# Performance work log

Measured on AMD Instinct MI355X. Metric: run time of the kernel, lower is better.

Reference implementation:

```python
import jax, jax.numpy as jnp
import numpy as np

D_MODEL = 16
D_STATE = 16
D_CONV = 4
EXPAND = 2
D_INNER = EXPAND * D_MODEL  # 32
DT_RANK = 1                 # ceil(d_model / 16)
H_MLP = 2 * D_MODEL         # MLP hidden = input_dim * 2
EPS = 1e-6
B, L = 16, 8192


def setup_inputs() -> dict:
    key = jax.random.key(0)
    ks = jax.random.split(key, 20)
    g = lambda i, shape, s: jax.random.normal(ks[i], shape, jnp.float32) * s
    # S4D-real init for A_log, as in mamba_ssm
    A_log = jnp.log(jnp.broadcast_to(jnp.arange(1, D_STATE + 1, dtype=jnp.float32), (D_INNER, D_STATE)))
    return {
        "x": jax.random.normal(ks[0], (B, L, D_MODEL), jnp.float32),
        "rms1_w": jnp.ones((D_MODEL,), jnp.float32),
        "in_proj_w": g(1, (D_MODEL, 2 * D_INNER), 0.25),
        "conv_w": g(2, (D_INNER, D_CONV), 0.3),
        "conv_b": g(3, (D_INNER,), 0.05),
        "x_proj_w": g(4, (D_INNER, DT_RANK + 2 * D_STATE), 0.2),
        "dt_proj_w": g(5, (DT_RANK, D_INNER), 0.5),
        "dt_proj_b": g(6, (D_INNER,), 0.1),
        "A_log": A_log,
        "D_skip": jnp.ones((D_INNER,), jnp.float32),
        "out_proj_w": g(7, (D_INNER, D_MODEL), 0.2),
        "rms2_w": jnp.ones((D_MODEL,), jnp.float32),
        "fc1_w": g(8, (D_MODEL, H_MLP), 0.25),
        "fc1_b": g(9, (H_MLP,), 0.05),
        "fc2_w": g(10, (H_MLP, H_MLP), 0.2),
        "fc2_b": g(11, (H_MLP,), 0.05),
        "fc3_w": g(12, (H_MLP, D_MODEL), 0.2),
        "fc3_b": g(13, (D_MODEL,), 0.05),
    }


def _rmsnorm(h, w):
    v = jnp.mean(h.astype(jnp.float32) ** 2, axis=-1, keepdims=True)
    return w * (h * jax.lax.rsqrt(v + EPS))


def _mamba(x0, in_proj_w, conv_w, conv_b, x_proj_w, dt_proj_w, dt_proj_b, A_log, D_skip, out_proj_w):
    b, l, _ = x0.shape
    xz = x0 @ in_proj_w                      # [B,L,2*Di]
    xm, z = jnp.split(xz, 2, axis=-1)        # each [B,L,Di]
    # causal depthwise conv1d (kernel D_CONV), padding d_conv-1, truncated to L
    xp = jnp.pad(xm, ((0, 0), (D_CONV - 1, 0), (0, 0)))
    xc = conv_b + sum(conv_w[:, k] * xp[:, k:k + l, :] for k in range(D_CONV))
    xc = jax.nn.silu(xc)
    # input-dependent dt, B, C
    proj = xc @ x_proj_w                     # [B,L,dt_rank+2*Ds]
    dt, Bm, Cm = jnp.split(proj, [DT_RANK, DT_RANK + D_STATE], axis=-1)
    dt = jax.nn.softplus(dt @ dt_proj_w + dt_proj_b)   # [B,L,Di]
    A = -jnp.exp(A_log)                      # [Di,Ds]
    deltaA = jnp.exp(dt[..., None] * A)                             # [B,L,Di,Ds]
    deltaBx = dt[..., None] * Bm[:, :, None, :] * xc[..., None]     # [B,L,Di,Ds]
    # sequential selective scan over time (time-major for lax.scan)
    def step(h, inputs):
        dA, dBx, C = inputs                  # [B,Di,Ds],[B,Di,Ds],[B,Ds]
        h = dA * h + dBx
        y = jnp.einsum('bds,bs->bd', h, C)
        return h, y
    h0 = jnp.zeros((b, D_INNER, D_STATE), xc.dtype)
    xs = (deltaA.transpose(1, 0, 2, 3), deltaBx.transpose(1, 0, 2, 3), Cm.transpose(1, 0, 2))
    _, ys = jax.lax.scan(step, h0, xs)       # [L,B,Di]
    y = ys.transpose(1, 0, 2) + D_skip * xc  # [B,L,Di]
    y = y * jax.nn.silu(z)
    return y @ out_proj_w                    # [B,L,Dm]


def reference(x, rms1_w, in_proj_w, conv_w, conv_b, x_proj_w, dt_proj_w, dt_proj_b,
              A_log, D_skip, out_proj_w, rms2_w, fc1_w, fc1_b, fc2_w, fc2_b, fc3_w, fc3_b):
    x0 = _rmsnorm(x, rms1_w)
    x1 = _mamba(x0, in_proj_w, conv_w, conv_b, x_proj_w, dt_proj_w, dt_proj_b, A_log, D_skip, out_proj_w)
    x = x1 + x
    x2 = _rmsnorm(x, rms2_w)
    h = jax.nn.relu(x2 @ fc1_w + fc1_b)
    h = jax.nn.relu(h @ fc2_w + fc2_b)
    x3 = h @ fc3_w + fc3_b
    return x + x3
```

## Files before the change

### kernel.cpp

```cpp
#include <hip/hip_runtime.h>

#define LSEQ 8192
#define NBAT 16
#define DMOD 16
#define DINN 32
#define DSTA 16
#define CL   32
#define NCH  (LSEQ / CL)
#define NCHT (NBAT * NCH)
#define NROWS (NBAT * LSEQ)
#define SUMN ((size_t)NCHT * 512)
#define NSEG 8
#define SEGC (NCH / NSEG)
#define RECU 800
#define LOG2E 1.44269504f

typedef __attribute__((ext_vector_type(8))) short bf16x8;
typedef __attribute__((ext_vector_type(4))) float f32x4;

__device__ __forceinline__ float fsilu(float v) { return v / (1.f + __expf(-v)); }
__device__ __forceinline__ float fsoftplus(float v) {
  return v > 20.f ? v : __logf(1.f + __expf(v));
}
__device__ __forceinline__ unsigned packbf(float a, float b) {
  unsigned r;
  asm("v_cvt_pk_bf16_f32 %0, %1, %2" : "=v"(r) : "v"(a), "v"(b));
  return r;
}
__device__ __forceinline__ short f2bf(float f) {
  return (short)(packbf(f, f) & 0xffffu);
}
__device__ __forceinline__ float bf2f(short s) {
  union { unsigned u; float f; } v;
  v.u = ((unsigned)(unsigned short)s) << 16;
  return v.f;
}
__device__ __forceinline__ float bflo(unsigned u) {
  union { unsigned a; float f; } v; v.a = u << 16; return v.f;
}
__device__ __forceinline__ float bfhi(unsigned u) {
  union { unsigned a; float f; } v; v.a = u & 0xffff0000u; return v.f;
}

__device__ __forceinline__ void load_x_row(const float* __restrict__ x, long r,
                                           float* __restrict__ xr) {
  const float4* xp = reinterpret_cast<const float4*>(x + r * DMOD);
  float4 v0 = xp[0], v1 = xp[1], v2 = xp[2], v3 = xp[3];
  xr[0] = v0.x; xr[1] = v0.y; xr[2] = v0.z; xr[3] = v0.w;
  xr[4] = v1.x; xr[5] = v1.y; xr[6] = v1.z; xr[7] = v1.w;
  xr[8] = v2.x; xr[9] = v2.y; xr[10] = v2.z; xr[11] = v2.w;
  xr[12] = v3.x; xr[13] = v3.y; xr[14] = v3.z; xr[15] = v3.w;
}

__device__ __forceinline__ f32x4 mm(bf16x8 a, bf16x8 b, f32x4 c) {
  return __builtin_amdgcn_mfma_f32_16x16x32_bf16(a, b, c, 0, 0, 0);
}
__device__ __forceinline__ bf16x8 bfrag(const float* __restrict__ W, int ldw,
                                        int coloff, int col, int kg, int kreal) {
  bf16x8 b = {0, 0, 0, 0, 0, 0, 0, 0};
#pragma unroll
  for (int e = 0; e < 8; e++) {
    int k = kg * 8 + e;
    if (k < kreal) b[e] = f2bf(W[k * ldw + coloff + col]);
  }
  return b;
}

__global__ __launch_bounds__(256) void k_prep(
    const float* __restrict__ x, const float* __restrict__ rms1w,
    const float* __restrict__ ipw, const float* __restrict__ cw,
    const float* __restrict__ cb, const float* __restrict__ xpw,
    const float* __restrict__ dtw, const float* __restrict__ dtb,
    const float* __restrict__ A_log, const float* __restrict__ Dskip,
    unsigned* __restrict__ rec, float* __restrict__ Pb,
    float* __restrict__ Hb) {
  __shared__ short xmv[67][36];
  __shared__ short x0b[64][40];
  __shared__ short xcb[64][40];
  int t = threadIdx.x;
  int lane = t & 63, wid = t >> 6;
  int col = lane & 15, kg = lane >> 4;
  long row0 = (long)blockIdx.x * 64;
  int l0 = (int)(row0 & (LSEQ - 1));
  const f32x4 zero4 = {0.f, 0.f, 0.f, 0.f};

  bf16x8 Bip0 = bfrag(ipw, 64, 0, col, kg, 16);
  bf16x8 Bip1 = bfrag(ipw, 64, 16, col, kg, 16);
  bf16x8 Bdt, Bb, Bc;
#pragma unroll
  for (int e = 0; e < 8; e++) {
    int k = kg * 8 + e;
    Bdt[e] = (col == 0) ? f2bf(xpw[k * 33]) : (short)0;
    Bb[e] = f2bf(xpw[k * 33 + 1 + col]);
    Bc[e] = f2bf(xpw[k * 33 + 17 + col]);
  }

  if (t < 128) {
    int row = t >> 1, hf = t & 1;
    const float4* xp =
        reinterpret_cast<const float4*>(x + (row0 + row) * DMOD + hf * 8);
    float4 v0 = xp[0], v1 = xp[1];
    float xr[8] = {v0.x, v0.y, v0.z, v0.w, v1.x, v1.y, v1.z, v1.w};
    float ss = 0.f;
#pragma unroll
    for (int i = 0; i < 8; i++) ss += xr[i] * xr[i];
    ss += __shfl_xor(ss, 1);
    float inv1 = rsqrtf(ss * (1.f / 16.f) + 1e-6f);
    unsigned u[4];
#pragma unroll
    for (int i = 0; i < 4; i++)
      u[i] = packbf(xr[2 * i] * inv1 * rms1w[hf * 8 + 2 * i],
                    xr[2 * i + 1] * inv1 * rms1w[hf * 8 + 2 * i + 1]);
    *reinterpret_cast<uint4*>(&x0b[row][hf * 8]) =
        make_uint4(u[0], u[1], u[2], u[3]);
  } else if (t < 224) {
    int h = (t - 128) >> 5, k = (t - 128) & 31;
    short v = 0;
    if (l0 != 0) {
      float xr[16];
      load_x_row(x, row0 - 3 + h, xr);
      float ss = 0.f;
#pragma unroll
      for (int i = 0; i < 16; i++) ss += xr[i] * xr[i];
      float inv1 = rsqrtf(ss * (1.f / 16.f) + 1e-6f);
      float acc = 0.f;
#pragma unroll
      for (int i = 0; i < 16; i++)
        acc = fmaf(xr[i] * inv1 * rms1w[i], ipw[i * 64 + k], acc);
      v = f2bf(acc);
    }
    xmv[h][k] = v;
  }
  __syncthreads();

  {
    int arow = wid * 16 + col;
    bf16x8 a = {0, 0, 0, 0, 0, 0, 0, 0};
    if (kg < 2) a = *reinterpret_cast<const bf16x8*>(&x0b[arow][kg * 8]);
    f32x4 m0 = mm(a, Bip0, zero4);
    f32x4 m1 = mm(a, Bip1, zero4);
    int orow = 3 + wid * 16 + kg * 4;
#pragma unroll
    for (int reg = 0; reg < 4; reg++) {
      unsigned p = packbf(m0[reg], m1[reg]);
      xmv[orow + reg][col] = (short)(p & 0xffffu);
      xmv[orow + reg][col + 16] = (short)(p >> 16);
    }
  }
  __syncthreads();

  {
    int row = t >> 2, q = t & 3;
    unsigned u[4];
#pragma unroll
    for (int dp = 0; dp < 4; dp++) {
      int d = q * 8 + dp * 2;
      float ce = cb[d], co = cb[d + 1];
#pragma unroll
      for (int k = 0; k < 4; k++) {
        unsigned xu = *reinterpret_cast<const unsigned*>(&xmv[row + k][d]);
        ce = fmaf(cw[d * 4 + k], bflo(xu), ce);
        co = fmaf(cw[(d + 1) * 4 + k], bfhi(xu), co);
      }
      u[dp] = packbf(fsilu(ce), fsilu(co));
    }
    *reinterpret_cast<uint4*>(&xcb[row][q * 8]) =
        make_uint4(u[0], u[1], u[2], u[3]);
  }
  __syncthreads();

  {
    int arow = wid * 16 + col;
    bf16x8 a2 = *reinterpret_cast<const bf16x8*>(&xcb[arow][kg * 8]);
    f32x4 pd = mm(a2, Bdt, zero4);
    f32x4 pb = mm(a2, Bb, zero4);
    f32x4 pc = mm(a2, Bc, zero4);
    int orow = wid * 16 + kg * 4;
#pragma unroll
    for (int reg = 0; reg < 4; reg++) {
      unsigned p = packbf(pb[reg], pc[reg]);
      xmv[orow + reg][col] = (short)(p & 0xffffu);
      xmv[orow + reg][16 + col] = (short)(p >> 16);
      if (col == 0) xmv[orow + reg][32] = f2bf(pd[reg]);
    }
  }
  __syncthreads();

  {
    int row = t >> 2, q = t & 3;
    float p0 = bf2f(xmv[row][32]);
    unsigned u[4];
#pragma unroll
    for (int dp = 0; dp < 4; dp++) {
      int d = q * 8 + dp * 2;
      u[dp] = packbf(fsoftplus(fmaf(p0, dtw[d], dtb[d])),
                     fsoftplus(fmaf(p0, dtw[d + 1], dtb[d + 1])));
    }
    *reinterpret_cast<uint4*>(&x0b[row][q * 8]) =
        make_uint4(u[0], u[1], u[2], u[3]);
  }
  __syncthreads();

  {
    int ch = t >> 7, b128 = t & 127;
    int d = b128 >> 2, s4 = (b128 & 3) << 2;
    float Ad0 = -__expf(A_log[d * 16 + s4 + 0]) * LOG2E;
    float Ad1 = -__expf(A_log[d * 16 + s4 + 1]) * LOG2E;
    float Ad2 = -__expf(A_log[d * 16 + s4 + 2]) * LOG2E;
    float Ad3 = -__expf(A_log[d * 16 + s4 + 3]) * LOG2E;
    float dskd = Dskip[d];
    bool w0 = (t & 3) == 0;
    float H0 = 0.f, H1 = 0.f, H2 = 0.f, H3 = 0.f, cum = 0.f;
#pragma unroll 4
    for (int li = 0; li < CL; li++) {
      int row = ch * CL + li;
      float dt = bf2f(x0b[row][d]);
      float xcv = bf2f(xcb[row][d]);
      float dx = dt * xcv;
      cum += dt;
      uint2 bu = *reinterpret_cast<const uint2*>(&xmv[row][s4]);
      uint2 cu = *reinterpret_cast<const uint2*>(&xmv[row][16 + s4]);
      float a;
      a = __builtin_amdgcn_exp2f(dt * Ad0); H0 = fmaf(a, H0, dx * bflo(bu.x));
      a = __builtin_amdgcn_exp2f(dt * Ad1); H1 = fmaf(a, H1, dx * bfhi(bu.x));
      a = __builtin_amdgcn_exp2f(dt * Ad2); H2 = fmaf(a, H2, dx * bflo(bu.y));
      a = __builtin_amdgcn_exp2f(dt * Ad3); H3 = fmaf(a, H3, dx * bfhi(bu.y));
      float py = bflo(cu.x) * H0;
      py = fmaf(bfhi(cu.x), H1, py);
      py = fmaf(bflo(cu.y), H2, py);
      py = fmaf(bfhi(cu.y), H3, py);
      py += __shfl_xor(py, 1);
      py += __shfl_xor(py, 2);
      if (w0) xcb[row][d] = f2bf(fmaf(dskd, xcv, py));
    }
    size_t sb_ = (size_t)(blockIdx.x * 2 + ch) * 512 + (size_t)(d * 16 + s4);
    *reinterpret_cast<float4*>(Pb + sb_) = make_float4(
        __builtin_amdgcn_exp2f(cum * Ad0), __builtin_amdgcn_exp2f(cum * Ad1),
        __builtin_amdgcn_exp2f(cum * Ad2), __builtin_amdgcn_exp2f(cum * Ad3));
    *reinterpret_cast<float4*>(Hb + sb_) = make_float4(H0, H1, H2, H3);
  }
  __syncthreads();

  {
    unsigned* rb0 = rec + (size_t)(blockIdx.x * 2) * RECU;
#pragma unroll
    for (int i = 0; i < 7; i++) {
      int idx = i * 256 + t;
      if (idx < 1600) {
        int ch = idx / 800;
        int rem = idx - ch * 800;
        int c = rem >> 5, l = rem & 31;
        int row = ch * 32 + l;
        unsigned val;
        if (c < 16)
          val = *reinterpret_cast<const unsigned*>(&xcb[row][2 * c]);
        else if (c < 24)
          val = *reinterpret_cast<const unsigned*>(&xmv[row][16 + 2 * (c - 16)]);
        else
          val = (unsigned)(unsigned short)xmv[row][32];
        rb0[ch * RECU + rem] = val;
      }
    }
  }
}

__global__ __launch_bounds__(256) void k_seg(float* __restrict__ Pb,
                                             float* __restrict__ Hb,
                                             float* __restrict__ segP,
                                             float* __restrict__ segH) {
  int g = blockIdx.x * 256 + threadIdx.x;
  int b = g >> 12;
  int rem = g & 4095;
  int seg = rem >> 9, st = rem & 511;
  size_t o = ((size_t)(b * NCH + seg * SEGC)) * 512 + st;
  float h = 0.f, p = 1.f;
#pragma unroll 4
  for (int c = 0; c < SEGC; c++) {
    float P = Pb[o], H = Hb[o];
    Pb[o] = p;
    Hb[o] = h;
    h = fmaf(P, h, H);
    p *= P;
    o += 512;
  }
  size_t so = (size_t)(b * NSEG + seg) * 512 + st;
  segP[so] = p;
  segH[so] = h;
}

__global__ __launch_bounds__(256) void k_carry(const float* __restrict__ segP,
                                               const float* __restrict__ segH,
                                               float* __restrict__ carry) {
  int g = blockIdx.x * 256 + threadIdx.x;
  int b = g >> 9, st = g & 511;
  float h = 0.f;
#pragma unroll
  for (int s = 0; s < NSEG; s++) {
    size_t so = (size_t)(b * NSEG + s) * 512 + st;
    carry[so] = h;
    h = fmaf(segP[so], h, segH[so]);
  }
}

__global__ __launch_bounds__(256) void k_mlp(
    const unsigned* __restrict__ rec, const float* __restrict__ x,
    const float* __restrict__ A_log, const float* __restrict__ Pb,
    const float* __restrict__ Hb, const float* __restrict__ carry,
    const float* __restrict__ dtw, const float* __restrict__ dtb,
    const float* __restrict__ rms1w, const float* __restrict__ ipw,
    const float* __restrict__ opw, const float* __restrict__ rms2w,
    const float* __restrict__ f1w, const float* __restrict__ f1b,
    const float* __restrict__ f2w, const float* __restrict__ f2b,
    const float* __restrict__ f3w, const float* __restrict__ f3b,
    float* __restrict__ out) {
  __shared__ float h0L[4 * 516];
  __shared__ float Ads[512];
  __shared__ short sbx[128][24];
  __shared__ short sby[128][40];
  int t = threadIdx.x, bc = blockIdx.x;
  long row0 = (long)bc * 128;

  Ads[t] = -__expf(A_log[t]) * LOG2E;
  Ads[256 + t] = -__expf(A_log[256 + t]) * LOG2E;
#pragma unroll
  for (int i = 0; i < 8; i++) {
    int idx = i * 256 + t;
    int chl = idx >> 9, st = idx & 511;
    int gc = bc * 4 + chl;
    size_t o = (size_t)gc * 512 + st;
    int b = gc >> 8, seg = (gc >> 5) & 7;
    h0L[chl * 516 + st] =
        fmaf(Pb[o], carry[(size_t)(b * NSEG + seg) * 512 + st], Hb[o]);
  }
  {
    int row = t >> 1, hf = t & 1;
    const float4* xp =
        reinterpret_cast<const float4*>(x + (row0 + row) * DMOD + hf * 8);
    float4 v0 = xp[0], v1 = xp[1];
    float xr[8] = {v0.x, v0.y, v0.z, v0.w, v1.x, v1.y, v1.z, v1.w};
    float ss = 0.f;
#pragma unroll
    for (int i = 0; i < 8; i++) ss += xr[i] * xr[i];
    ss += __shfl_xor(ss, 1);
    float inv1 = rsqrtf(ss * (1.f / 16.f) + 1e-6f);
    unsigned u[4];
#pragma unroll
    for (int i = 0; i < 4; i++)
      u[i] = packbf(xr[2 * i] * inv1 * rms1w[hf * 8 + 2 * i],
                    xr[2 * i + 1] * inv1 * rms1w[hf * 8 + 2 * i + 1]);
    *reinterpret_cast<uint4*>(&sbx[t >> 1][hf * 8]) =
        make_uint4(u[0], u[1], u[2], u[3]);
  }
  __syncthreads();

  {
    int ch = t >> 6, half = (t >> 5) & 1, l = t & 31;
    const unsigned* rb = rec + (size_t)(bc * 4 + ch) * RECU;
    float Cv[16];
#pragma unroll
    for (int c = 0; c < 8; c++) {
      unsigned u = rb[(16 + c) * 32 + l];
      Cv[2 * c] = bflo(u);
      Cv[2 * c + 1] = bfhi(u);
    }
    float p0 = bflo(rb[24 * 32 + l]);
    const float* h0c = &h0L[ch * 516];
    int row = ch * 32 + l;
#pragma unroll
    for (int cc = 0; cc < 8; cc++) {
      int c = half * 8 + cc;
      int d0 = 2 * c, d1 = 2 * c + 1;
      float cd0 = fsoftplus(fmaf(p0, dtw[d0], dtb[d0]));
      float cd1 = fsoftplus(fmaf(p0, dtw[d1], dtb[d1]));
#pragma unroll
      for (int dl = 1; dl < 32; dl <<= 1) {
        float u0 = __shfl_up(cd0, dl, 32);
        float u1 = __shfl_up(cd1, dl, 32);
        if (l >= dl) { cd0 += u0; cd1 += u1; }
      }
      unsigned yu = rb[c * 32 + l];
      float acc0 = bflo(yu), acc1 = bfhi(yu);
      int dof0 = d0 * 16, dof1 = d1 * 16;
#pragma unroll
      for (int s = 0; s < 16; s++) {
        float e0 = __builtin_amdgcn_exp2f(Ads[dof0 + s] * cd0);
        float e1 = __builtin_amdgcn_exp2f(Ads[dof1 + s] * cd1);
        acc0 = fmaf(e0 * Cv[s], h0c[dof0 + s], acc0);
        acc1 = fmaf(e1 * Cv[s], h0c[dof1 + s], acc1);
      }
      *reinterpret_cast<unsigned*>(&sby[row][2 * c]) = packbf(acc0, acc1);
    }
  }
  __syncthreads();

  {
    int lane = t & 63, w = t >> 6;
    int col = lane & 15, kg = lane >> 4;
    bf16x8 Bz0 = bfrag(ipw + 32, 64, 0, col, kg, 16);
    bf16x8 Bz1 = bfrag(ipw + 32, 64, 16, col, kg, 16);
    bf16x8 Bop = bfrag(opw, 16, 0, col, kg, 32);
    bf16x8 Bf1_0 = bfrag(f1w, 32, 0, col, kg, 16);
    bf16x8 Bf1_1 = bfrag(f1w, 32, 16, col, kg, 16);
    bf16x8 Bf2_0 = bfrag(f2w, 32, 0, col, kg, 32);
    bf16x8 Bf2_1 = bfrag(f2w, 32, 16, col, kg, 32);
    bf16x8 Bf3 = bfrag(f3w, 16, 0, col, kg, 32);
    float b1_0 = f1b[col], b1_1 = f1b[16 + col];
    float b2_0 = f2b[col], b2_1 = f2b[16 + col];
    float b3c = f3b[col], rw2 = rms2w[col];
    const f32x4 zero4 = {0.f, 0.f, 0.f, 0.f};
#pragma unroll 1
    for (int rt = 0; rt < 2; rt++) {
      int tile0 = w * 32 + rt * 16;
      bf16x8 ax0 = {0, 0, 0, 0, 0, 0, 0, 0};
      if (kg < 2) ax0 = *reinterpret_cast<const bf16x8*>(&sbx[tile0 + col][kg * 8]);
      f32x4 zf0 = mm(ax0, Bz0, zero4);
      f32x4 zf1 = mm(ax0, Bz1, zero4);
#pragma unroll
      for (int reg = 0; reg < 4; reg++) {
        int lrow = tile0 + kg * 4 + reg;
        float y0 = bf2f(sby[lrow][col]);
        float y1 = bf2f(sby[lrow][16 + col]);
        unsigned p = packbf(y0 * fsilu(zf0[reg]), y1 * fsilu(zf1[reg]));
        sby[lrow][col] = (short)(p & 0xffffu);
        sby[lrow][16 + col] = (short)(p >> 16);
      }
      bf16x8 ayo = *reinterpret_cast<const bf16x8*>(&sby[tile0 + col][kg * 8]);
      f32x4 x1f = mm(ayo, Bop, zero4);
      float xres[4];
#pragma unroll
      for (int reg = 0; reg < 4; reg++) {
        long grow = row0 + tile0 + kg * 4 + reg;
        xres[reg] = x1f[reg] + x[grow * 16 + col];
      }
#pragma unroll
      for (int reg = 0; reg < 4; reg++) {
        float ss = xres[reg] * xres[reg];
        ss += __shfl_xor(ss, 1);
        ss += __shfl_xor(ss, 2);
        ss += __shfl_xor(ss, 4);
        ss += __shfl_xor(ss, 8);
        float inv2 = rsqrtf(ss * (1.f / 16.f) + 1e-6f);
        sby[tile0 + kg * 4 + reg][col] = f2bf(xres[reg] * inv2 * rw2);
      }
      bf16x8 ax2 = {0, 0, 0, 0, 0, 0, 0, 0};
      if (kg < 2) ax2 = *reinterpret_cast<const bf16x8*>(&sby[tile0 + col][kg * 8]);
      f32x4 h1f0 = mm(ax2, Bf1_0, zero4);
      f32x4 h1f1 = mm(ax2, Bf1_1, zero4);
#pragma unroll
      for (int reg = 0; reg < 4; reg++) {
        int lrow = tile0 + kg * 4 + reg;
        unsigned p = packbf(fmaxf(h1f0[reg] + b1_0, 0.f),
                            fmaxf(h1f1[reg] + b1_1, 0.f));
        sby[lrow][col] = (short)(p & 0xffffu);
        sby[lrow][16 + col] = (short)(p >> 16);
      }
      bf16x8 ah1 = *reinterpret_cast<const bf16x8*>(&sby[tile0 + col][kg * 8]);
      f32x4 h2f0 = mm(ah1, Bf2_0, zero4);
      f32x4 h2f1 = mm(ah1, Bf2_1, zero4);
#pragma unroll
      for (int reg = 0; reg < 4; reg++) {
        int lrow = tile0 + kg * 4 + reg;
        unsigned p = packbf(fmaxf(h2f0[reg] + b2_0, 0.f),
                            fmaxf(h2f1[reg] + b2_1, 0.f));
        sby[lrow][col] = (short)(p & 0xffffu);
        sby[lrow][16 + col] = (short)(p >> 16);
      }
      bf16x8 ah2 = *reinterpret_cast<const bf16x8*>(&sby[tile0 + col][kg * 8]);
      f32x4 x3f = mm(ah2, Bf3, zero4);
#pragma unroll
      for (int reg = 0; reg < 4; reg++) {
        long grow = row0 + tile0 + kg * 4 + reg;
        out[grow * 16 + col] = xres[reg] + x3f[reg] + b3c;
      }
    }
  }
}

extern "C" void kernel_launch(void* const* d_in, const int* in_sizes, int n_in,
                              void* d_out, int out_size, void* d_ws,
                              size_t ws_size, hipStream_t stream) {
  const float* x = (const float*)d_in[0];
  const float* rms1w = (const float*)d_in[1];
  const float* ipw = (const float*)d_in[2];
  const float* cw = (const float*)d_in[3];
  const float* cb = (const float*)d_in[4];
  const float* xpw = (const float*)d_in[5];
  const float* dtw = (const float*)d_in[6];
  const float* dtb = (const float*)d_in[7];
  const float* A_log = (const float*)d_in[8];
  const float* Dskip = (const float*)d_in[9];
  const float* opw = (const float*)d_in[10];
  const float* rms2w = (const float*)d_in[11];
  const float* f1w = (const float*)d_in[12];
  const float* f1b = (const float*)d_in[13];
  const float* f2w = (const float*)d_in[14];
  const float* f2b = (const float*)d_in[15];
  const float* f3w = (const float*)d_in[16];
  const float* f3b = (const float*)d_in[17];
  float* out = (float*)d_out;

  unsigned* rec = (unsigned*)d_ws;
  float* Pb = (float*)(rec + (size_t)NCHT * RECU);
  float* Hb = Pb + SUMN;
  float* segP = Hb + SUMN;
  float* segH = segP + NBAT * NSEG * 512;
  float* carry = segH + NBAT * NSEG * 512;

  hipLaunchKernelGGL(k_prep, dim3(NROWS / 64), dim3(256), 0, stream, x, rms1w,
                     ipw, cw, cb, xpw, dtw, dtb, A_log, Dskip, rec, Pb, Hb);
  hipLaunchKernelGGL(k_seg, dim3(256), dim3(256), 0, stream, Pb, Hb, segP,
                     segH);
  hipLaunchKernelGGL(k_carry, dim3(32), dim3(256), 0, stream, segP, segH,
                     carry);
  hipLaunchKernelGGL(k_mlp, dim3(NROWS / 128), dim3(256), 0, stream, rec, x,
                     A_log, Pb, Hb, carry, dtw, dtb, rms1w, ipw, opw, rms2w,
                     f1w, f1b, f2w, f2b, f3w, f3b, out);
}
```

Measured before the change: 84.67 us.

## Make each wavefront own one chunk so block barriers become compiler fences

k_prep and k_mlp are restructured so every 64-lane wavefront processes its own 32-row chunk in private shared-memory slices. Most __syncthreads barriers become compiler-only memory fences, relying on in-wave lockstep execution. The scan gives each lane 8 states instead of 4, which halves the shuffle reduction but doubles per-lane serial work. The k_prep grid is halved, and the change risks lower parallelism in the scan plus correctness that depends on wave-synchronous LDS ordering.

```diff
diff --git a/kernel.cpp b/kernel.cpp
--- a/kernel.cpp
+++ b/kernel.cpp
@@ -14,6 +14,7 @@
 #define SEGC (NCH / NSEG)
 #define RECU 800
 #define LOG2E 1.44269504f
+#define FENCE() asm volatile("" ::: "memory")
 
 typedef __attribute__((ext_vector_type(8))) short bf16x8;
 typedef __attribute__((ext_vector_type(4))) float f32x4;
@@ -74,14 +75,15 @@
     const float* __restrict__ A_log, const float* __restrict__ Dskip,
     unsigned* __restrict__ rec, float* __restrict__ Pb,
     float* __restrict__ Hb) {
-  __shared__ short xmv[67][36];
-  __shared__ short x0b[64][40];
-  __shared__ short xcb[64][40];
+  __shared__ short XM[4][35][36];
+  __shared__ short X0[4][32][32];
+  __shared__ short XC[4][32][40];
   int t = threadIdx.x;
-  int lane = t & 63, wid = t >> 6;
-  int col = lane & 15, kg = lane >> 4;
-  long row0 = (long)blockIdx.x * 64;
-  int l0 = (int)(row0 & (LSEQ - 1));
+  int l = t & 63, wid = t >> 6;
+  int col = l & 15, kg = l >> 4;
+  int chunk = blockIdx.x * 4 + wid;
+  long row0 = (long)chunk * CL;
+  bool first = (chunk & (NCH - 1)) == 0;
   const f32x4 zero4 = {0.f, 0.f, 0.f, 0.f};
 
   bf16x8 Bip0 = bfrag(ipw, 64, 0, col, kg, 16);
@@ -95,8 +97,8 @@
     Bc[e] = f2bf(xpw[k * 33 + 17 + col]);
   }
 
-  if (t < 128) {
-    int row = t >> 1, hf = t & 1;
+  {
+    int row = l >> 1, hf = l & 1;
     const float4* xp =
         reinterpret_cast<const float4*>(x + (row0 + row) * DMOD + hf * 8);
     float4 v0 = xp[0], v1 = xp[1];
@@ -111,154 +113,174 @@
     for (int i = 0; i < 4; i++)
       u[i] = packbf(xr[2 * i] * inv1 * rms1w[hf * 8 + 2 * i],
                     xr[2 * i + 1] * inv1 * rms1w[hf * 8 + 2 * i + 1]);
-    *reinterpret_cast<uint4*>(&x0b[row][hf * 8]) =
+    *reinterpret_cast<uint4*>(&X0[wid][row][hf * 8]) =
         make_uint4(u[0], u[1], u[2], u[3]);
-  } else if (t < 224) {
-    int h = (t - 128) >> 5, k = (t - 128) & 31;
-    short v = 0;
-    if (l0 != 0) {
+  }
+  if (l < 48) {
+    int h = l >> 4, k2 = (l & 15) * 2;
+    float a0 = 0.f, a1 = 0.f;
+    if (!first) {
       float xr[16];
       load_x_row(x, row0 - 3 + h, xr);
       float ss = 0.f;
 #pragma unroll
       for (int i = 0; i < 16; i++) ss += xr[i] * xr[i];
       float inv1 = rsqrtf(ss * (1.f / 16.f) + 1e-6f);
-      float acc = 0.f;
-#pragma unroll
-      for (int i = 0; i < 16; i++)
-        acc = fmaf(xr[i] * inv1 * rms1w[i], ipw[i * 64 + k], acc);
-      v = f2bf(acc);
-    }
-    xmv[h][k] = v;
-  }
-  __syncthreads();
-
-  {
-    int arow = wid * 16 + col;
+#pragma unroll
+      for (int i = 0; i < 16; i++) {
+        float x0i = xr[i] * inv1 * rms1w[i];
+        a0 = fmaf(x0i, ipw[i * 64 + k2], a0);
+        a1 = fmaf(x0i, ipw[i * 64 + k2 + 1], a1);
+      }
+    }
+    *reinterpret_cast<unsigned*>(&XM[wid][h][k2]) = packbf(a0, a1);
+  }
+  FENCE();
+
+#pragma unroll
+  for (int rt = 0; rt < 2; rt++) {
+    int arow = rt * 16 + col;
     bf16x8 a = {0, 0, 0, 0, 0, 0, 0, 0};
-    if (kg < 2) a = *reinterpret_cast<const bf16x8*>(&x0b[arow][kg * 8]);
+    if (kg < 2) a = *reinterpret_cast<const bf16x8*>(&X0[wid][arow][kg * 8]);
     f32x4 m0 = mm(a, Bip0, zero4);
     f32x4 m1 = mm(a, Bip1, zero4);
-    int orow = 3 + wid * 16 + kg * 4;
+    int orow = 3 + rt * 16 + kg * 4;
 #pragma unroll
     for (int reg = 0; reg < 4; reg++) {
       unsigned p = packbf(m0[reg], m1[reg]);
-      xmv[orow + reg][col] = (short)(p & 0xffffu);
-      xmv[orow + reg][col + 16] = (short)(p >> 16);
-    }
-  }
-  __syncthreads();
-
-  {
-    int row = t >> 2, q = t & 3;
-    unsigned u[4];
-#pragma unroll
-    for (int dp = 0; dp < 4; dp++) {
-      int d = q * 8 + dp * 2;
+      XM[wid][orow + reg][col] = (short)(p & 0xffffu);
+      XM[wid][orow + reg][col + 16] = (short)(p >> 16);
+    }
+  }
+  FENCE();
+
+  {
+    int row = l >> 1, hf = l & 1;
+    unsigned u[8];
+#pragma unroll
+    for (int dp = 0; dp < 8; dp++) {
+      int d = hf * 16 + dp * 2;
       float ce = cb[d], co = cb[d + 1];
 #pragma unroll
       for (int k = 0; k < 4; k++) {
-        unsigned xu = *reinterpret_cast<const unsigned*>(&xmv[row + k][d]);
+        unsigned xu = *reinterpret_cast<const unsigned*>(&XM[wid][row + k][d]);
         ce = fmaf(cw[d * 4 + k], bflo(xu), ce);
         co = fmaf(cw[(d + 1) * 4 + k], bfhi(xu), co);
       }
       u[dp] = packbf(fsilu(ce), fsilu(co));
     }
-    *reinterpret_cast<uint4*>(&xcb[row][q * 8]) =
+    *reinterpret_cast<uint4*>(&XC[wid][row][hf * 16]) =
         make_uint4(u[0], u[1], u[2], u[3]);
-  }
-  __syncthreads();
-
-  {
-    int arow = wid * 16 + col;
-    bf16x8 a2 = *reinterpret_cast<const bf16x8*>(&xcb[arow][kg * 8]);
+    *reinterpret_cast<uint4*>(&XC[wid][row][hf * 16 + 8]) =
+        make_uint4(u[4], u[5], u[6], u[7]);
+  }
+  FENCE();
+
+#pragma unroll
+  for (int rt = 0; rt < 2; rt++) {
+    int arow = rt * 16 + col;
+    bf16x8 a2 = *reinterpret_cast<const bf16x8*>(&XC[wid][arow][kg * 8]);
     f32x4 pd = mm(a2, Bdt, zero4);
     f32x4 pb = mm(a2, Bb, zero4);
     f32x4 pc = mm(a2, Bc, zero4);
-    int orow = wid * 16 + kg * 4;
+    int orow = 3 + rt * 16 + kg * 4;
 #pragma unroll
     for (int reg = 0; reg < 4; reg++) {
       unsigned p = packbf(pb[reg], pc[reg]);
-      xmv[orow + reg][col] = (short)(p & 0xffffu);
-      xmv[orow + reg][16 + col] = (short)(p >> 16);
-      if (col == 0) xmv[orow + reg][32] = f2bf(pd[reg]);
-    }
-  }
-  __syncthreads();
-
-  {
-    int row = t >> 2, q = t & 3;
-    float p0 = bf2f(xmv[row][32]);
-    unsigned u[4];
-#pragma unroll
-    for (int dp = 0; dp < 4; dp++) {
-      int d = q * 8 + dp * 2;
+      XM[wid][orow + reg][col] = (short)(p & 0xffffu);
+      XM[wid][orow + reg][16 + col] = (short)(p >> 16);
+      if (col == 0) XM[wid][orow + reg][32] = f2bf(pd[reg]);
+    }
+  }
+  FENCE();
+
+  {
+    int row = l >> 1, hf = l & 1;
+    float p0 = bf2f(XM[wid][3 + row][32]);
+    unsigned u[8];
+#pragma unroll
+    for (int dp = 0; dp < 8; dp++) {
+      int d = hf * 16 + dp * 2;
       u[dp] = packbf(fsoftplus(fmaf(p0, dtw[d], dtb[d])),
                      fsoftplus(fmaf(p0, dtw[d + 1], dtb[d + 1])));
     }
-    *reinterpret_cast<uint4*>(&x0b[row][q * 8]) =
+    *reinterpret_cast<uint4*>(&X0[wid][row][hf * 16]) =
         make_uint4(u[0], u[1], u[2], u[3]);
-  }
-  __syncthreads();
-
-  {
-    int ch = t >> 7, b128 = t & 127;
-    int d = b128 >> 2, s4 = (b128 & 3) << 2;
-    float Ad0 = -__expf(A_log[d * 16 + s4 + 0]) * LOG2E;
-    float Ad1 = -__expf(A_log[d * 16 + s4 + 1]) * LOG2E;
-    float Ad2 = -__expf(A_log[d * 16 + s4 + 2]) * LOG2E;
-    float Ad3 = -__expf(A_log[d * 16 + s4 + 3]) * LOG2E;
+    *reinterpret_cast<uint4*>(&X0[wid][row][hf * 16 + 8]) =
+        make_uint4(u[4], u[5], u[6], u[7]);
+  }
+  FENCE();
+
+  {
+    int d = l >> 1, sh = (l & 1) * 8;
+    float4 alo = *reinterpret_cast<const float4*>(A_log + d * DSTA + sh);
+    float4 ahi = *reinterpret_cast<const float4*>(A_log + d * DSTA + sh + 4);
+    float Ad[8] = {-__expf(alo.x) * LOG2E, -__expf(alo.y) * LOG2E,
+                   -__expf(alo.z) * LOG2E, -__expf(alo.w) * LOG2E,
+                   -__expf(ahi.x) * LOG2E, -__expf(ahi.y) * LOG2E,
+                   -__expf(ahi.z) * LOG2E, -__expf(ahi.w) * LOG2E};
     float dskd = Dskip[d];
-    bool w0 = (t & 3) == 0;
-    float H0 = 0.f, H1 = 0.f, H2 = 0.f, H3 = 0.f, cum = 0.f;
+    float H[8] = {0.f, 0.f, 0.f, 0.f, 0.f, 0.f, 0.f, 0.f};
+    float cum = 0.f;
+    bool wy = (l & 1) == 0;
 #pragma unroll 4
     for (int li = 0; li < CL; li++) {
-      int row = ch * CL + li;
-      float dt = bf2f(x0b[row][d]);
-      float xcv = bf2f(xcb[row][d]);
+      float dt = bf2f(X0[wid][li][d]);
+      float xcv = bf2f(XC[wid][li][d]);
       float dx = dt * xcv;
       cum += dt;
-      uint2 bu = *reinterpret_cast<const uint2*>(&xmv[row][s4]);
-      uint2 cu = *reinterpret_cast<const uint2*>(&xmv[row][16 + s4]);
+      uint2 bu0 = *reinterpret_cast<const uint2*>(&XM[wid][3 + li][sh]);
+      uint2 bu1 = *reinterpret_cast<const uint2*>(&XM[wid][3 + li][sh + 4]);
+      uint2 cu0 = *reinterpret_cast<const uint2*>(&XM[wid][3 + li][16 + sh]);
+      uint2 cu1 = *reinterpret_cast<const uint2*>(&XM[wid][3 + li][16 + sh + 4]);
       float a;
-      a = __builtin_amdgcn_exp2f(dt * Ad0); H0 = fmaf(a, H0, dx * bflo(bu.x));
-      a = __builtin_amdgcn_exp2f(dt * Ad1); H1 = fmaf(a, H1, dx * bfhi(bu.x));
-      a = __builtin_amdgcn_exp2f(dt * Ad2); H2 = fmaf(a, H2, dx * bflo(bu.y));
-      a = __builtin_amdgcn_exp2f(dt * Ad3); H3 = fmaf(a, H3, dx * bfhi(bu.y));
-      float py = bflo(cu.x) * H0;
-      py = fmaf(bfhi(cu.x), H1, py);
-      py = fmaf(bflo(cu.y), H2, py);
-      py = fmaf(bfhi(cu.y), H3, py);
-      py += __shfl_xor(py, 1);
-      py += __shfl_xor(py, 2);
-      if (w0) xcb[row][d] = f2bf(fmaf(dskd, xcv, py));
-    }
-    size_t sb_ = (size_t)(blockIdx.x * 2 + ch) * 512 + (size_t)(d * 16 + s4);
+      a = __builtin_amdgcn_exp2f(dt * Ad[0]); H[0] = fmaf(a, H[0], dx * bflo(bu0.x));
+      a = __builtin_amdgcn_exp2f(dt * Ad[1]); H[1] = fmaf(a, H[1], dx * bfhi(bu0.x));
+      a = __builtin_amdgcn_exp2f(dt * Ad[2]); H[2] = fmaf(a, H[2], dx * bflo(bu0.y));
+      a = __builtin_amdgcn_exp2f(dt * Ad[3]); H[3] = fmaf(a, H[3], dx * bfhi(bu0.y));
+      a = __builtin_amdgcn_exp2f(dt * Ad[4]); H[4] = fmaf(a, H[4], dx * bflo(bu1.x));
+      a = __builtin_amdgcn_exp2f(dt * Ad[5]); H[5] = fmaf(a, H[5], dx * bfhi(bu1.x));
+      a = __builtin_amdgcn_exp2f(dt * Ad[6]); H[6] = fmaf(a, H[6], dx * bflo(bu1.y));
+      a = __builtin_amdgcn_exp2f(dt * Ad[7]); H[7] = fmaf(a, H[7], dx * bfhi(bu1.y));
+      float y = bflo(cu0.x) * H[0];
+      y = fmaf(bfhi(cu0.x), H[1], y);
+      y = fmaf(bflo(cu0.y), H[2], y);
+      y = fmaf(bfhi(cu0.y), H[3], y);
+      y = fmaf(bflo(cu1.x), H[4], y);
+      y = fmaf(bfhi(cu1.x), H[5], y);
+      y = fmaf(bflo(cu1.y), H[6], y);
+      y = fmaf(bfhi(cu1.y), H[7], y);
+      y += __shfl_xor(y, 1);
+      if (wy) XC[wid][li][d] = f2bf(fmaf(dskd, xcv, y));
+    }
+    size_t sb_ = (size_t)chunk * 512 + (size_t)(l * 8);
     *reinterpret_cast<float4*>(Pb + sb_) = make_float4(
-        __builtin_amdgcn_exp2f(cum * Ad0), __builtin_amdgcn_exp2f(cum * Ad1),
-        __builtin_amdgcn_exp2f(cum * Ad2), __builtin_amdgcn_exp2f(cum * Ad3));
-    *reinterpret_cast<float4*>(Hb + sb_) = make_float4(H0, H1, H2, H3);
-  }
-  __syncthreads();
-
-  {
-    unsigned* rb0 = rec + (size_t)(blockIdx.x * 2) * RECU;
-#pragma unroll
-    for (int i = 0; i < 7; i++) {
-      int idx = i * 256 + t;
-      if (idx < 1600) {
-        int ch = idx / 800;
-        int rem = idx - ch * 800;
-        int c = rem >> 5, l = rem & 31;
-        int row = ch * 32 + l;
+        __builtin_amdgcn_exp2f(cum * Ad[0]), __builtin_amdgcn_exp2f(cum * Ad[1]),
+        __builtin_amdgcn_exp2f(cum * Ad[2]), __builtin_amdgcn_exp2f(cum * Ad[3]));
+    *reinterpret_cast<float4*>(Pb + sb_ + 4) = make_float4(
+        __builtin_amdgcn_exp2f(cum * Ad[4]), __builtin_amdgcn_exp2f(cum * Ad[5]),
+        __builtin_amdgcn_exp2f(cum * Ad[6]), __builtin_amdgcn_exp2f(cum * Ad[7]));
+    *reinterpret_cast<float4*>(Hb + sb_) = make_float4(H[0], H[1], H[2], H[3]);
+    *reinterpret_cast<float4*>(Hb + sb_ + 4) = make_float4(H[4], H[5], H[6], H[7]);
+  }
+  FENCE();
+
+  {
+    unsigned* rb = rec + (size_t)chunk * RECU;
+#pragma unroll
+    for (int i = 0; i < 13; i++) {
+      int idx = i * 64 + l;
+      if (idx < 800) {
+        int c = idx >> 5, r = idx & 31;
         unsigned val;
         if (c < 16)
-          val = *reinterpret_cast<const unsigned*>(&xcb[row][2 * c]);
+          val = *reinterpret_cast<const unsigned*>(&XC[wid][r][2 * c]);
         else if (c < 24)
-          val = *reinterpret_cast<const unsigned*>(&xmv[row][16 + 2 * (c - 16)]);
+          val = *reinterpret_cast<const unsigned*>(
+              &XM[wid][3 + r][16 + 2 * (c - 16)]);
         else
-          val = (unsigned)(unsigned short)xmv[row][32];
-        rb0[ch * RECU + rem] = val;
+          val = (unsigned)(unsigned short)XM[wid][3 + r][32];
+        rb[idx] = val;
       }
     }
   }
@@ -313,27 +335,36 @@
     const float* __restrict__ f2w, const float* __restrict__ f2b,
     const float* __restrict__ f3w, const float* __restrict__ f3b,
     float* __restrict__ out) {
-  __shared__ float h0L[4 * 516];
   __shared__ float Ads[512];
-  __shared__ short sbx[128][24];
-  __shared__ short sby[128][40];
-  int t = threadIdx.x, bc = blockIdx.x;
-  long row0 = (long)bc * 128;
+  __shared__ float h0w[4][512];
+  __shared__ short sbx[4][32][24];
+  __shared__ short sby[4][32][40];
+  int t = threadIdx.x;
+  int l = t & 63, wid = t >> 6;
+  int gc = blockIdx.x * 4 + wid;
+  long row0 = (long)gc * CL;
 
   Ads[t] = -__expf(A_log[t]) * LOG2E;
   Ads[256 + t] = -__expf(A_log[256 + t]) * LOG2E;
-#pragma unroll
-  for (int i = 0; i < 8; i++) {
-    int idx = i * 256 + t;
-    int chl = idx >> 9, st = idx & 511;
-    int gc = bc * 4 + chl;
-    size_t o = (size_t)gc * 512 + st;
+  {
+    size_t o = (size_t)gc * 512 + (size_t)(l * 8);
     int b = gc >> 8, seg = (gc >> 5) & 7;
-    h0L[chl * 516 + st] =
-        fmaf(Pb[o], carry[(size_t)(b * NSEG + seg) * 512 + st], Hb[o]);
-  }
-  {
-    int row = t >> 1, hf = t & 1;
+    size_t co = (size_t)(b * NSEG + seg) * 512 + (size_t)(l * 8);
+    float4 pv0 = *reinterpret_cast<const float4*>(Pb + o);
+    float4 pv1 = *reinterpret_cast<const float4*>(Pb + o + 4);
+    float4 hv0 = *reinterpret_cast<const float4*>(Hb + o);
+    float4 hv1 = *reinterpret_cast<const float4*>(Hb + o + 4);
+    float4 cv0 = *reinterpret_cast<const float4*>(carry + co);
+    float4 cv1 = *reinterpret_cast<const float4*>(carry + co + 4);
+    *reinterpret_cast<float4*>(&h0w[wid][l * 8]) =
+        make_float4(fmaf(pv0.x, cv0.x, hv0.x), fmaf(pv0.y, cv0.y, hv0.y),
+                    fmaf(pv0.z, cv0.z, hv0.z), fmaf(pv0.w, cv0.w, hv0.w));
+    *reinterpret_cast<float4*>(&h0w[wid][l * 8 + 4]) =
+        make_float4(fmaf(pv1.x, cv1.x, hv1.x), fmaf(pv1.y, cv1.y, hv1.y),
+                    fmaf(pv1.z, cv1.z, hv1.z), fmaf(pv1.w, cv1.w, hv1.w));
+  }
+  {
+    int row = l >> 1, hf = l & 1;
     const float4* xp =
         reinterpret_cast<const float4*>(x + (row0 + row) * DMOD + hf * 8);
     float4 v0 = xp[0], v1 = xp[1];
@@ -348,24 +379,23 @@
     for (int i = 0; i < 4; i++)
       u[i] = packbf(xr[2 * i] * inv1 * rms1w[hf * 8 + 2 * i],
                     xr[2 * i + 1] * inv1 * rms1w[hf * 8 + 2 * i + 1]);
-    *reinterpret_cast<uint4*>(&sbx[t >> 1][hf * 8]) =
+    *reinterpret_cast<uint4*>(&sbx[wid][row][hf * 8]) =
         make_uint4(u[0], u[1], u[2], u[3]);
   }
   __syncthreads();
 
   {
-    int ch = t >> 6, half = (t >> 5) & 1, l = t & 31;
-    const unsigned* rb = rec + (size_t)(bc * 4 + ch) * RECU;
+    int half = l >> 5, r = l & 31;
+    const unsigned* rb = rec + (size_t)gc * RECU;
     float Cv[16];
 #pragma unroll
     for (int c = 0; c < 8; c++) {
-      unsigned u = rb[(16 + c) * 32 + l];
+      unsigned u = rb[(16 + c) * 32 + r];
       Cv[2 * c] = bflo(u);
       Cv[2 * c + 1] = bfhi(u);
     }
-    float p0 = bflo(rb[24 * 32 + l]);
-    const float* h0c = &h0L[ch * 516];
-    int row = ch * 32 + l;
+    float p0 = bflo(rb[24 * 32 + r]);
+    const float* h0c = h0w[wid];
 #pragma unroll
     for (int cc = 0; cc < 8; cc++) {
       int c = half * 8 + cc;
@@ -376,9 +406,9 @@
       for (int dl = 1; dl < 32; dl <<= 1) {
         float u0 = __shfl_up(cd0, dl, 32);
         float u1 = __shfl_up(cd1, dl, 32);
-        if (l >= dl) { cd0 += u0; cd1 += u1; }
-      }
-      unsigned yu = rb[c * 32 + l];
+        if (r >= dl) { cd0 += u0; cd1 += u1; }
+      }
+      unsigned yu = rb[c * 32 + r];
       float acc0 = bflo(yu), acc1 = bfhi(yu);
       int dof0 = d0 * 16, dof1 = d1 * 16;
 #pragma unroll
@@ -388,14 +418,13 @@
         acc0 = fmaf(e0 * Cv[s], h0c[dof0 + s], acc0);
         acc1 = fmaf(e1 * Cv[s], h0c[dof1 + s], acc1);
       }
-      *reinterpret_cast<unsigned*>(&sby[row][2 * c]) = packbf(acc0, acc1);
-    }
-  }
-  __syncthreads();
-
-  {
-    int lane = t & 63, w = t >> 6;
-    int col = lane & 15, kg = lane >> 4;
+      *reinterpret_cast<unsigned*>(&sby[wid][r][2 * c]) = packbf(acc0, acc1);
+    }
+  }
+  FENCE();
+
+  {
+    int col = l & 15, kg = l >> 4;
     bf16x8 Bz0 = bfrag(ipw + 32, 64, 0, col, kg, 16);
     bf16x8 Bz1 = bfrag(ipw + 32, 64, 16, col, kg, 16);
     bf16x8 Bop = bfrag(opw, 16, 0, col, kg, 32);
@@ -410,21 +439,24 @@
     const f32x4 zero4 = {0.f, 0.f, 0.f, 0.f};
 #pragma unroll 1
     for (int rt = 0; rt < 2; rt++) {
-      int tile0 = w * 32 + rt * 16;
+      int tile0 = rt * 16;
       bf16x8 ax0 = {0, 0, 0, 0, 0, 0, 0, 0};
-      if (kg < 2) ax0 = *reinterpret_cast<const bf16x8*>(&sbx[tile0 + col][kg * 8]);
+      if (kg < 2)
+        ax0 = *reinterpret_cast<const bf16x8*>(&sbx[wid][tile0 + col][kg * 8]);
       f32x4 zf0 = mm(ax0, Bz0, zero4);
       f32x4 zf1 = mm(ax0, Bz1, zero4);
 #pragma unroll
       for (int reg = 0; reg < 4; reg++) {
         int lrow = tile0 + kg * 4 + reg;
-        float y0 = bf2f(sby[lrow][col]);
-        float y1 = bf2f(sby[lrow][16 + col]);
+        float y0 = bf2f(sby[wid][lrow][col]);
+        float y1 = bf2f(sby[wid][lrow][16 + col]);
         unsigned p = packbf(y0 * fsilu(zf0[reg]), y1 * fsilu(zf1[reg]));
-        sby[lrow][col] = (short)(p & 0xffffu);
-        sby[lrow][16 + col] = (short)(p >> 16);
-      }
-      bf16x8 ayo = *reinterpret_cast<const bf16x8*>(&sby[tile0 + col][kg * 8]);
+        sby[wid][lrow][col] = (short)(p & 0xffffu);
+        sby[wid][lrow][16 + col] = (short)(p >> 16);
+      }
+      FENCE();
+      bf16x8 ayo =
+          *reinterpret_cast<const bf16x8*>(&sby[wid][tile0 + col][kg * 8]);
       f32x4 x1f = mm(ayo, Bop, zero4);
       float xres[4];
 #pragma unroll
@@ -440,10 +472,12 @@
         ss += __shfl_xor(ss, 4);
         ss += __shfl_xor(ss, 8);
         float inv2 = rsqrtf(ss * (1.f / 16.f) + 1e-6f);
-        sby[tile0 + kg * 4 + reg][col] = f2bf(xres[reg] * inv2 * rw2);
-      }
+        sby[wid][tile0 + kg * 4 + reg][col] = f2bf(xres[reg] * inv2 * rw2);
+      }
+      FENCE();
       bf16x8 ax2 = {0, 0, 0, 0, 0, 0, 0, 0};
-      if (kg < 2) ax2 = *reinterpret_cast<const bf16x8*>(&sby[tile0 + col][kg * 8]);
+      if (kg < 2)
+        ax2 = *reinterpret_cast<const bf16x8*>(&sby[wid][tile0 + col][kg * 8]);
       f32x4 h1f0 = mm(ax2, Bf1_0, zero4);
       f32x4 h1f1 = mm(ax2, Bf1_1, zero4);
 #pragma unroll
@@ -451,10 +485,12 @@
         int lrow = tile0 + kg * 4 + reg;
         unsigned p = packbf(fmaxf(h1f0[reg] + b1_0, 0.f),
                             fmaxf(h1f1[reg] + b1_1, 0.f));
-        sby[lrow][col] = (short)(p & 0xffffu);
-        sby[lrow][16 + col] = (short)(p >> 16);
-      }
-      bf16x8 ah1 = *reinterpret_cast<const bf16x8*>(&sby[tile0 + col][kg * 8]);
+        sby[wid][lrow][col] = (short)(p & 0xffffu);
+        sby[wid][lrow][16 + col] = (short)(p >> 16);
+      }
+      FENCE();
+      bf16x8 ah1 =
+          *reinterpret_cast<const bf16x8*>(&sby[wid][tile0 + col][kg * 8]);
       f32x4 h2f0 = mm(ah1, Bf2_0, zero4);
       f32x4 h2f1 = mm(ah1, Bf2_1, zero4);
 #pragma unroll
@@ -462,16 +498,19 @@
         int lrow = tile0 + kg * 4 + reg;
         unsigned p = packbf(fmaxf(h2f0[reg] + b2_0, 0.f),
                             fmaxf(h2f1[reg] + b2_1, 0.f));
-        sby[lrow][col] = (short)(p & 0xffffu);
-        sby[lrow][16 + col] = (short)(p >> 16);
-      }
-      bf16x8 ah2 = *reinterpret_cast<const bf16x8*>(&sby[tile0 + col][kg * 8]);
+        sby[wid][lrow][col] = (short)(p & 0xffffu);
+        sby[wid][lrow][16 + col] = (short)(p >> 16);
+      }
+      FENCE();
+      bf16x8 ah2 =
+          *reinterpret_cast<const bf16x8*>(&sby[wid][tile0 + col][kg * 8]);
       f32x4 x3f = mm(ah2, Bf3, zero4);
 #pragma unroll
       for (int reg = 0; reg < 4; reg++) {
         long grow = row0 + tile0 + kg * 4 + reg;
         out[grow * 16 + col] = xres[reg] + x3f[reg] + b3c;
       }
+      FENCE();
     }
   }
 }
@@ -506,7 +545,7 @@
   float* segH = segP + NBAT * NSEG * 512;
   float* carry = segH + NBAT * NSEG * 512;
 
-  hipLaunchKernelGGL(k_prep, dim3(NROWS / 64), dim3(256), 0, stream, x, rms1w,
+  hipLaunchKernelGGL(k_prep, dim3(NROWS / 128), dim3(256), 0, stream, x, rms1w,
                      ipw, cw, cb, xpw, dtw, dtb, A_log, Dskip, rec, Pb, Hb);
   hipLaunchKernelGGL(k_seg, dim3(256), dim3(256), 0, stream, Pb, Hb, segP,
                      segH);
```

New measurement: 76.72 us, median of 2. -9.4%, faster.
